# Kernel optimization log

Hardware: AMD Instinct MI355X
Metric: run time of the kernel (lower is better)

The kernel has to match this reference:

```python
import jax, jax.numpy as jnp
import numpy as np

N = 50000      # nodes
E = 800000     # edges
D = 256        # embed_dim
H = 8          # num_heads
HD = D // H    # head_dim = 32
F = 4 * D      # feedforward_dim = 1024
SCALE = D ** -0.5  # note: module scales by embed_dim**-0.5, not head_dim
EPS = 1e-5


def setup_inputs() -> dict:
    key = jax.random.key(0)
    ks = jax.random.split(key, 10)
    x = jax.random.normal(ks[0], (N, D), dtype=jnp.float32)
    edge_indices = jax.random.randint(ks[1], (2, E), 0, N, dtype=jnp.int32)
    s = 0.02
    return {
        "x": x,
        "edge_indices": edge_indices,
        "w_qkv": jax.random.normal(ks[2], (D, 3 * D), dtype=jnp.float32) * s,
        "b_qkv": jnp.zeros((3 * D,), dtype=jnp.float32),
        "ln1_g": jnp.ones((D,), dtype=jnp.float32),
        "ln1_b": jnp.zeros((D,), dtype=jnp.float32),
        "ln2_g": jnp.ones((D,), dtype=jnp.float32),
        "ln2_b": jnp.zeros((D,), dtype=jnp.float32),
        "w1": jax.random.normal(ks[3], (D, F), dtype=jnp.float32) * s,
        "b1": jnp.zeros((F,), dtype=jnp.float32),
        "w2": jax.random.normal(ks[4], (F, D), dtype=jnp.float32) * s,
        "b2": jnp.zeros((D,), dtype=jnp.float32),
    }


def _layer_norm(x, g, b):
    m = jnp.mean(x, axis=-1, keepdims=True)
    v = jnp.mean((x - m) ** 2, axis=-1, keepdims=True)
    return (x - m) * jax.lax.rsqrt(v + EPS) * g + b


def _self_attention(x, edge_indices, w_qkv, b_qkv):
    qkv = (x @ w_qkv + b_qkv).reshape(N, H, 3 * HD)
    q, k, v = qkv[..., :HD], qkv[..., HD:2 * HD], qkv[..., 2 * HD:]
    rows, cols = edge_indices[0], edge_indices[1]
    # per-edge, per-head attention logits: [E, H]
    alpha = jnp.einsum('ehd,ehd->eh', q[rows], k[cols]) * SCALE
    # sparse softmax over each row (destination node) segment
    m = jax.ops.segment_max(alpha, rows, num_segments=N)       # [N, H]
    ea = jnp.exp(alpha - m[rows])                              # [E, H]
    denom = jax.ops.segment_sum(ea, rows, num_segments=N)      # [N, H]
    w = ea / denom[rows]                                       # [E, H]
    # per-head SpMM: out[r] += w_e * v[c]  -> [N, H, HD]
    out = jax.ops.segment_sum(w[:, :, None] * v[cols], rows, num_segments=N)
    return out.reshape(N, D)


def reference(x, edge_indices, w_qkv, b_qkv, ln1_g, ln1_b, ln2_g, ln2_b, w1, b1, w2, b2):
    # post-norm (norm_first=False), dropout=0
    x = _layer_norm(x + _self_attention(x, edge_indices, w_qkv, b_qkv), ln1_g, ln1_b)
    ffn = jax.nn.relu(x @ w1 + b1) @ w2 + b2
    x = _layer_norm(x + ffn, ln2_g, ln2_b)
    return x
```

## Files before the change

kernel.cpp:

```cpp
#include <hip/hip_runtime.h>
#include <hip/hip_bf16.h>

#define N_NODES 50000
#define E_EDGES 800000
#define D_MODEL 256
#define H_HEADS 8
#define HDIM    32
#define F_FFN   1024
#define ATT_SCALE 0.0625f
#define LN_EPS  1e-5f
#define NB_SCAN 196

typedef __attribute__((ext_vector_type(8))) short bf16x8;
typedef __attribute__((ext_vector_type(8))) unsigned short u16x8;
typedef __attribute__((ext_vector_type(4))) float f32x4;

__device__ __forceinline__ float bf2f(__hip_bfloat16 v) { return __bfloat162float(v); }
__device__ __forceinline__ __hip_bfloat16 f2bf(float v) { return __float2bfloat16(v); }
__device__ __forceinline__ unsigned short bfbits(float f) {
    __hip_bfloat16 h = __float2bfloat16(f);
    return *reinterpret_cast<unsigned short*>(&h);
}

__device__ __forceinline__ void unpack_bf8(uint4 u, float* f) {
    f[0] = __uint_as_float(u.x << 16); f[1] = __uint_as_float(u.x & 0xFFFF0000u);
    f[2] = __uint_as_float(u.y << 16); f[3] = __uint_as_float(u.y & 0xFFFF0000u);
    f[4] = __uint_as_float(u.z << 16); f[5] = __uint_as_float(u.z & 0xFFFF0000u);
    f[6] = __uint_as_float(u.w << 16); f[7] = __uint_as_float(u.w & 0xFFFF0000u);
}

template<int CTRL>
__device__ __forceinline__ float dpp_add(float v) {
    int t = __builtin_amdgcn_update_dpp(0, __float_as_int(v), CTRL, 0xF, 0xF, true);
    return v + __int_as_float(t);
}

__device__ __forceinline__ void load_lds16(const void* g, void* l) {
    __builtin_amdgcn_global_load_lds(
        (const __attribute__((address_space(1))) unsigned*)g,
        (__attribute__((address_space(3))) unsigned*)l, 16, 0, 0);
}

#define WAITV(N) asm volatile("s_waitcnt vmcnt(" #N ")" ::: "memory")
#define SBAR()   { __builtin_amdgcn_sched_barrier(0); __builtin_amdgcn_s_barrier(); \
                   __builtin_amdgcn_sched_barrier(0); }


#define PREP_E   E_EDGES
#define PREP_X   3200000
#define PREP_WQ  (768 * 256)
#define PREP_W1  (1024 * 256)
#define PREP_W2  (256 * 1024)
#define PREP_BQ  768
#define PREP_B1  1024
#define PREP_TOT (PREP_E + PREP_X + PREP_WQ + PREP_W1 + PREP_W2 + PREP_BQ + PREP_B1)
__global__ void prep_kernel(const int* __restrict__ rows, unsigned* __restrict__ counts,
                            const float* __restrict__ x, unsigned short* __restrict__ xb,
                            const float* __restrict__ wq, __hip_bfloat16* __restrict__ wtq,
                            const float* __restrict__ w1, __hip_bfloat16* __restrict__ wt1,
                            const float* __restrict__ w2, __hip_bfloat16* __restrict__ wt2,
                            const float* __restrict__ bq, float* __restrict__ bqp,
                            const float* __restrict__ b1, float* __restrict__ b1p) {
    int i = blockIdx.x * blockDim.x + threadIdx.x;
    if (i < PREP_E) {
        atomicAdd(&counts[rows[i]], 1u);
        return;
    }
    i -= PREP_E;
    if (i < PREP_X) {
        float4 v = reinterpret_cast<const float4*>(x)[i];
        ushort4 o;
        o.x = bfbits(v.x); o.y = bfbits(v.y); o.z = bfbits(v.z); o.w = bfbits(v.w);
        reinterpret_cast<ushort4*>(xb)[i] = o;
        return;
    }
    i -= PREP_X;
    if (i < PREP_WQ) {
        int n = i >> 8, k = i & 255;
        int s = n >> 8, prel = n & 255;
        int d = (prel & 192) + ((prel & 15) << 2) + ((prel >> 4) & 3);
        int co = (d >> 5) * 96 + s * 32 + (d & 31);
        wtq[i] = f2bf(wq[(size_t)k * 768 + co]);
        return;
    }
    i -= PREP_WQ;
    if (i < PREP_W1) {
        int n = i >> 8, k = i & 255;
        int f = (n & ~63) + ((n & 15) << 2) + ((n >> 4) & 3);
        wt1[i] = f2bf(w1[(size_t)k * 1024 + f]);
        return;
    }
    i -= PREP_W1;
    if (i < PREP_W2) {
        int n = i >> 10, k = i & 1023;
        wt2[i] = f2bf(w2[(size_t)k * 256 + n]);
        return;
    }
    i -= PREP_W2;
    if (i < PREP_BQ) {
        int s = i >> 8, prel = i & 255;
        int d = (prel & 192) + ((prel & 15) << 2) + ((prel >> 4) & 3);
        bqp[i] = bq[(d >> 5) * 96 + s * 32 + (d & 31)];
        return;
    }
    i -= PREP_BQ;
    if (i < PREP_B1) {
        int f = (i & ~63) + ((i & 15) << 2) + ((i >> 4) & 3);
        b1p[i] = b1[f];
        return;
    }
}

template<bool RELU, int EPI, int KT>
__global__ __launch_bounds__(256)
void mfma_gemm(const __hip_bfloat16* __restrict__ A,
               const __hip_bfloat16* __restrict__ Wt,
               const float* __restrict__ bias,
               __hip_bfloat16* __restrict__ outp,
               __hip_bfloat16* __restrict__ qb,
               unsigned char* __restrict__ kv8,
               int M, int Ncols) {
    __shared__ short Al[3][128 * 32];
    __shared__ short Bl[3][128 * 32];
    const int t = threadIdx.x;
    const int wave = t >> 6, lane = t & 63;

    unsigned flat = blockIdx.y * gridDim.x + blockIdx.x;
    unsigned nwg = gridDim.x * gridDim.y;
    unsigned q8 = nwg >> 3, r8 = nwg & 7;
    unsigned xcd = flat & 7, pos = flat >> 3;
    unsigned wg = (xcd < r8) ? (xcd * (q8 + 1) + pos)
                             : (r8 * (q8 + 1) + (xcd - r8) * q8 + pos);
    const int m0 = (int)(wg / gridDim.x) * 128;
    const int n0 = (int)(wg % gridDim.x) * 128;

    const int wr = wave >> 1, wc = wave & 1;

    const int srow = lane >> 2;
    const int skp  = (lane & 3) ^ ((lane >> 3) & 3);
    const int c0 = wave * 2;
    int ar0 = m0 + c0 * 16 + srow;      if (ar0 >= M) ar0 = M - 1;
    int ar1 = m0 + c0 * 16 + 16 + srow; if (ar1 >= M) ar1 = M - 1;
    const __hip_bfloat16* ga0 = A + (size_t)ar0 * KT + skp * 8;
    const __hip_bfloat16* ga1 = A + (size_t)ar1 * KT + skp * 8;
    const __hip_bfloat16* gb0 = Wt + (size_t)(n0 + c0 * 16 + srow) * KT + skp * 8;
    const __hip_bfloat16* gb1 = Wt + (size_t)(n0 + c0 * 16 + 16 + srow) * KT + skp * 8;

    const int lh = lane & 15, q = lane >> 4;
    const int qs = q ^ ((lane >> 1) & 3);
    const short* faB = &Al[0][(wr * 64 + lh) * 32 + qs * 8];
    const short* fbB = &Bl[0][(wc * 64 + lh) * 32 + qs * 8];

    f32x4 acc[4][4] = {};

#define GSTAGE(B)                                    \
    load_lds16(ga0, &Al[B][c0 * 512]);               \
    load_lds16(ga1, &Al[B][c0 * 512 + 512]);         \
    load_lds16(gb0, &Bl[B][c0 * 512]);               \
    load_lds16(gb1, &Bl[B][c0 * 512 + 512]);         \
    ga0 += 32; ga1 += 32; gb0 += 32; gb1 += 32;

#define GSTEP(FA, FB)                                                       \
    {                                                                       \
        bf16x8 af[4], bfr[4];                                               \
        _Pragma("unroll")                                                   \
        for (int i = 0; i < 4; i++) {                                       \
            af[i]  = *reinterpret_cast<const bf16x8*>((FA) + i * 16 * 32);  \
            bfr[i] = *reinterpret_cast<const bf16x8*>((FB) + i * 16 * 32);  \
        }                                                                   \
        _Pragma("unroll")                                                   \
        for (int mi = 0; mi < 4; mi++)                                      \
            _Pragma("unroll")                                               \
            for (int nj = 0; nj < 4; nj++)                                  \
                acc[mi][nj] = __builtin_amdgcn_mfma_f32_16x16x32_bf16(      \
                    af[mi], bfr[nj], acc[mi][nj], 0, 0, 0);                 \
    }

    constexpr int ns = KT >> 5;
    GSTAGE(0)
    GSTAGE(1)
#pragma unroll
    for (int s = 0; s < ns; ++s) {
        if (s < ns - 1) { WAITV(4); } else { WAITV(0); }
        SBAR();
        if (s + 2 < ns) {
            switch ((s + 2) % 3) {
                case 0: { GSTAGE(0) } break;
                case 1: { GSTAGE(1) } break;
                default: { GSTAGE(2) } break;
            }
        }
        const short* fa = faB + (s % 3) * 4096;
        const short* fb = fbB + (s % 3) * 4096;
        GSTEP(fa, fb)
    }
#undef GSTAGE
#undef GSTEP

    const int B = n0 + wc * 64;
    const int gnbase = B + lh;
    float bv[4];
#pragma unroll
    for (int nj = 0; nj < 4; nj++) bv[nj] = bias[gnbase + nj * 16];

    if (EPI == 0) {
        const int sec = B >> 8;
        const int c = ((B & 255) >> 6) * 16 + lh;
#pragma unroll
        for (int mi = 0; mi < 4; mi++) {
            int gmb = m0 + wr * 64 + mi * 16 + q * 4;
#pragma unroll
            for (int r = 0; r < 4; r++) {
                int gm = gmb + r;
                if (gm >= M) continue;
                float v0 = acc[mi][0][r] + bv[0];
                float v1 = acc[mi][1][r] + bv[1];
                float v2 = acc[mi][2][r] + bv[2];
                float v3 = acc[mi][3][r] + bv[3];
                if (sec == 0) {
                    ushort4 o;
                    o.x = bfbits(v0); o.y = bfbits(v1); o.z = bfbits(v2); o.w = bfbits(v3);
                    *reinterpret_cast<ushort4*>(qb + (size_t)gm * 256 + c * 4) = o;
                } else {
                    unsigned u = (unsigned)__builtin_amdgcn_cvt_pk_fp8_f32(v0, v1, 0, false);
                    u = (unsigned)__builtin_amdgcn_cvt_pk_fp8_f32(v2, v3, (int)u, true);
                    *reinterpret_cast<unsigned*>(
                        kv8 + (size_t)gm * 512 + c * 8 + (sec == 1 ? 0 : 4)) = u;
                }
            }
        }
    } else {
        const int cb = B + lh * 4;
#pragma unroll
        for (int mi = 0; mi < 4; mi++) {
            int gmb = m0 + wr * 64 + mi * 16 + q * 4;
#pragma unroll
            for (int r = 0; r < 4; r++) {
                int gm = gmb + r;
                if (gm >= M) continue;
                float v0 = acc[mi][0][r] + bv[0];
                float v1 = acc[mi][1][r] + bv[1];
                float v2 = acc[mi][2][r] + bv[2];
                float v3 = acc[mi][3][r] + bv[3];
                if (RELU) {
                    v0 = fmaxf(v0, 0.f); v1 = fmaxf(v1, 0.f);
                    v2 = fmaxf(v2, 0.f); v3 = fmaxf(v3, 0.f);
                }
                ushort4 o;
                o.x = bfbits(v0); o.y = bfbits(v1); o.z = bfbits(v2); o.w = bfbits(v3);
                *reinterpret_cast<ushort4*>(outp + (size_t)gm * Ncols + cb) = o;
            }
        }
    }
}

__global__ __launch_bounds__(512)
void ffn2_ln_kernel(const __hip_bfloat16* __restrict__ A,
                    const __hip_bfloat16* __restrict__ Wt,
                    const float* __restrict__ bias,
                    const __hip_bfloat16* __restrict__ resid,
                    const float* __restrict__ g, const float* __restrict__ bb,
                    float* __restrict__ out, int M) {
    __shared__ short LDS[2][(64 + 256) * 32];
    const int t = threadIdx.x;
    const int wave = t >> 6, lane = t & 63;
    const int m0 = blockIdx.x * 64;
    const int wr = wave >> 2, wc = wave & 3;

    const int srow = lane >> 2;
    const int skp  = (lane & 3) ^ ((lane >> 3) & 3);

    const __hip_bfloat16* gsrc0; int loff0;
    const __hip_bfloat16* gsrc1; int loff1;
    const __hip_bfloat16* gsrc2; int loff2;
    {
#define STAGE_INIT(GS, LO, C)                                            \
        if ((C) < 4) {                                                   \
            int r_ = m0 + (C) * 16 + srow; if (r_ >= M) r_ = M - 1;      \
            GS = A + (size_t)r_ * 1024 + skp * 8;                        \
            LO = (C) * 512;                                              \
        } else {                                                         \
            GS = Wt + (size_t)(((C) - 4) * 16 + srow) * 1024 + skp * 8;  \
            LO = 2048 + ((C) - 4) * 512;                                 \
        }
        STAGE_INIT(gsrc0, loff0, wave)
        STAGE_INIT(gsrc1, loff1, wave + 8)
        int c2 = (wave < 4) ? wave + 16 : 16;
        STAGE_INIT(gsrc2, loff2, c2)
#undef STAGE_INIT
    }

    const int lh = lane & 15, q = lane >> 4;
    const int qs = q ^ ((lane >> 1) & 3);
    const short* fa0 = &LDS[0][(wr * 32 + lh) * 32 + qs * 8];
    const short* fb0 = &LDS[0][2048 + (wc * 64 + lh) * 32 + qs * 8];
    const short* fa1 = &LDS[1][(wr * 32 + lh) * 32 + qs * 8];
    const short* fb1 = &LDS[1][2048 + (wc * 64 + lh) * 32 + qs * 8];

    f32x4 acc[2][4] = {};

#define FFN2_STAGE(BUF)                                      \
    load_lds16(gsrc0, &LDS[BUF][loff0]);                     \
    load_lds16(gsrc1, &LDS[BUF][loff1]);                     \
    if (wave < 4) load_lds16(gsrc2, &LDS[BUF][loff2]);       \
    gsrc0 += 32; gsrc1 += 32; gsrc2 += 32;

#define FFN2_STEP(FA, FB)                                                   \
    {                                                                       \
        bf16x8 af[2], bfr[4];                                               \
        _Pragma("unroll")                                                   \
        for (int i = 0; i < 2; i++)                                         \
            af[i] = *reinterpret_cast<const bf16x8*>((FA) + i * 16 * 32);   \
        _Pragma("unroll")                                                   \
        for (int i = 0; i < 4; i++)                                         \
            bfr[i] = *reinterpret_cast<const bf16x8*>((FB) + i * 16 * 32);  \
        _Pragma("unroll")                                                   \
        for (int mi = 0; mi < 2; mi++)                                      \
            _Pragma("unroll")                                               \
            for (int nj = 0; nj < 4; nj++)                                  \
                acc[mi][nj] = __builtin_amdgcn_mfma_f32_16x16x32_bf16(      \
                    af[mi], bfr[nj], acc[mi][nj], 0, 0, 0);                 \
    }

    FFN2_STAGE(0)
    __syncthreads();

    for (int s = 0; s < 32; s += 2) {
        FFN2_STAGE(1)
        FFN2_STEP(fa0, fb0)
        __syncthreads();
        if (s < 30) { FFN2_STAGE(0) }
        FFN2_STEP(fa1, fb1)
        __syncthreads();
    }
#undef FFN2_STAGE
#undef FFN2_STEP

    const int colbase = wc * 64 + lh;
    float bv[4], gv[4], bbv[4];
#pragma unroll
    for (int nj = 0; nj < 4; nj++) {
        bv[nj]  = bias[colbase + nj * 16];
        gv[nj]  = g[colbase + nj * 16];
        bbv[nj] = bb[colbase + nj * 16];
    }

    float ps[2][4], pq[2][4];
#pragma unroll
    for (int mi = 0; mi < 2; mi++) {
#pragma unroll
        for (int r = 0; r < 4; r++) {
            int gm = m0 + wr * 32 + mi * 16 + q * 4 + r;
            int rgm = (gm < M) ? gm : M - 1;
            float s = 0.f, s2 = 0.f;
#pragma unroll
            for (int nj = 0; nj < 4; nj++) {
                float v = acc[mi][nj][r] + bv[nj]
                        + bf2f(resid[(size_t)rgm * 256 + colbase + nj * 16]);
                acc[mi][nj][r] = v;
                s += v; s2 += v * v;
            }
            ps[mi][r] = s; pq[mi][r] = s2;
        }
    }
#pragma unroll
    for (int off = 1; off <= 8; off <<= 1) {
#pragma unroll
        for (int mi = 0; mi < 2; mi++)
#pragma unroll
            for (int r = 0; r < 4; r++) {
                ps[mi][r] += __shfl_xor(ps[mi][r], off);
                pq[mi][r] += __shfl_xor(pq[mi][r], off);
            }
    }
    float* rs = (float*)(&LDS[0][0]);
    float* rq = rs + 256;
    if (lh == 0) {
#pragma unroll
        for (int mi = 0; mi < 2; mi++)
#pragma unroll
            for (int r = 0; r < 4; r++) {
                int m = wr * 32 + mi * 16 + q * 4 + r;
                rs[m * 4 + wc] = ps[mi][r];
                rq[m * 4 + wc] = pq[mi][r];
            }
    }
    __syncthreads();

#pragma unroll
    for (int mi = 0; mi < 2; mi++) {
#pragma unroll
        for (int r = 0; r < 4; r++) {
            int m = wr * 32 + mi * 16 + q * 4 + r;
            int gm = m0 + m;
            if (gm >= M) continue;
            float4 rsv = *reinterpret_cast<const float4*>(&rs[m * 4]);
            float4 rqv = *reinterpret_cast<const float4*>(&rq[m * 4]);
            float S  = (rsv.x + rsv.y) + (rsv.z + rsv.w);
            float S2 = (rqv.x + rqv.y) + (rqv.z + rqv.w);
            float mean = S * (1.f / (float)D_MODEL);
            float var  = S2 * (1.f / (float)D_MODEL) - mean * mean;
            float inv  = rsqrtf(var + LN_EPS);
#pragma unroll
            for (int nj = 0; nj < 4; nj++)
                out[(size_t)gm * 256 + colbase + nj * 16] =
                    (acc[mi][nj][r] - mean) * inv * gv[nj] + bbv[nj];
        }
    }
}

__global__ void scan_blk_kernel(const unsigned* __restrict__ counts,
                                unsigned* __restrict__ offs, unsigned* __restrict__ bsum) {
    __shared__ unsigned sh[256];
    int t = threadIdx.x;
    int i = blockIdx.x * 256 + t;
    unsigned v = (i < N_NODES) ? counts[i] : 0u;
    sh[t] = v;
    __syncthreads();
#pragma unroll
    for (int off = 1; off < 256; off <<= 1) {
        unsigned u = (t >= off) ? sh[t - off] : 0u;
        __syncthreads();
        sh[t] += u;
        __syncthreads();
    }
    if (i < N_NODES) offs[i] = sh[t] - v;
    if (t == 255) bsum[blockIdx.x] = sh[255];
}

__global__ void scan_top_kernel(const unsigned* __restrict__ bsum, unsigned* __restrict__ bpre) {
    __shared__ unsigned sh[256];
    int t = threadIdx.x;
    unsigned v = (t < NB_SCAN) ? bsum[t] : 0u;
    sh[t] = v;
    __syncthreads();
#pragma unroll
    for (int off = 1; off < 256; off <<= 1) {
        unsigned u = (t >= off) ? sh[t - off] : 0u;
        __syncthreads();
        sh[t] += u;
        __syncthreads();
    }
    if (t < NB_SCAN) bpre[t] = sh[t] - v;
    if (t == NB_SCAN - 1) bpre[NB_SCAN] = sh[t];
}

__global__ void scatter_kernel(const int* __restrict__ rows, const int* __restrict__ cols,
                               const unsigned* __restrict__ offsets,
                               const unsigned* __restrict__ bpre,
                               unsigned* __restrict__ cursor,
                               int* __restrict__ scol) {
    int e = blockIdx.x * blockDim.x + threadIdx.x;
    if (e >= E_EDGES) return;
    int r = rows[e];
    unsigned idx = atomicAdd(&cursor[r], 1u);
    scol[offsets[r] + bpre[r >> 8] + idx] = cols[e];
}

__global__ __launch_bounds__(128)
void att_agg_kernel(const __hip_bfloat16* __restrict__ qb,
                    const unsigned char* __restrict__ kv8,
                    const unsigned* __restrict__ offsets,
                    const unsigned* __restrict__ bpre,
                    const int* __restrict__ scol,
                    const __hip_bfloat16* __restrict__ xres,
                    const float* __restrict__ g, const float* __restrict__ bb,
                    __hip_bfloat16* __restrict__ xn) {
    int n = blockIdx.x * 2 + (threadIdx.x >> 6);
    if (n >= N_NODES) return;
    const int lam = threadIdx.x & 63;
    const int hl  = lam & 31;
    const int sel = lam >> 5;
    const unsigned hlb = hl * 16;
    unsigned beg = offsets[n] + bpre[n >> 8];
    unsigned end = (n + 1 == N_NODES) ? bpre[NB_SCAN]
                                      : offsets[n + 1] + bpre[(n + 1) >> 8];

    float qv[8];
    {
        uint4 u = *reinterpret_cast<const uint4*>(qb + (size_t)n * 256 + hl * 8);
        unpack_bf8(u, qv);
#pragma unroll
        for (int i = 0; i < 8; i++) qv[i] *= ATT_SCALE;
    }

    float acc[8] = {};
    float l = 0.f;

#define PAIR_BODY(W, VMUL)                                                      \
    {                                                                           \
        auto k01 = __builtin_amdgcn_cvt_pk_f32_fp8((int)(W).x, false);          \
        auto k23 = __builtin_amdgcn_cvt_pk_f32_fp8((int)(W).x, true);           \
        auto k45 = __builtin_amdgcn_cvt_pk_f32_fp8((int)(W).z, false);          \
        auto k67 = __builtin_amdgcn_cvt_pk_f32_fp8((int)(W).z, true);           \
        float sv = qv[0] * k01[0] + qv[1] * k01[1] + qv[2] * k23[0]             \
                 + qv[3] * k23[1] + qv[4] * k45[0] + qv[5] * k45[1]             \
                 + qv[6] * k67[0] + qv[7] * k67[1];                             \
        sv = dpp_add<0xB1>(sv);                                                 \
        sv = dpp_add<0x4E>(sv);                                                 \
        float pv = __expf(sv) * (VMUL);                                         \
        l += pv;                                                                \
        auto v01 = __builtin_amdgcn_cvt_pk_f32_fp8((int)(W).y, false);          \
        auto v23 = __builtin_amdgcn_cvt_pk_f32_fp8((int)(W).y, true);           \
        auto v45 = __builtin_amdgcn_cvt_pk_f32_fp8((int)(W).w, false);          \
        auto v67 = __builtin_amdgcn_cvt_pk_f32_fp8((int)(W).w, true);           \
        acc[0] += pv * v01[0]; acc[1] += pv * v01[1];                           \
        acc[2] += pv * v23[0]; acc[3] += pv * v23[1];                           \
        acc[4] += pv * v45[0]; acc[5] += pv * v45[1];                           \
        acc[6] += pv * v67[0]; acc[7] += pv * v67[1];                           \
    }

    unsigned e = beg;
    unsigned oA = 0, oB = 0, oC = 0, oD = 0;
    if (e + 8 <= end) {
        oA = ((unsigned)scol[e + sel])     << 9;
        oB = ((unsigned)scol[e + 2 + sel]) << 9;
        oC = ((unsigned)scol[e + 4 + sel]) << 9;
        oD = ((unsigned)scol[e + 6 + sel]) << 9;
    }
    while (e + 8 <= end) {
        uint4 wa = *reinterpret_cast<const uint4*>(kv8 + (oA + hlb));
        uint4 wb = *reinterpret_cast<const uint4*>(kv8 + (oB + hlb));
        uint4 wc = *reinterpret_cast<const uint4*>(kv8 + (oC + hlb));
        uint4 wd = *reinterpret_cast<const uint4*>(kv8 + (oD + hlb));
        e += 8;
        if (e + 8 <= end) {
            oA = ((unsigned)scol[e + sel])     << 9;
            oB = ((unsigned)scol[e + 2 + sel]) << 9;
            oC = ((unsigned)scol[e + 4 + sel]) << 9;
            oD = ((unsigned)scol[e + 6 + sel]) << 9;
        }
        PAIR_BODY(wa, 1.0f)
        PAIR_BODY(wb, 1.0f)
        PAIR_BODY(wc, 1.0f)
        PAIR_BODY(wd, 1.0f)
    }
    for (; e + 2 <= end; e += 2) {
        unsigned o0 = ((unsigned)scol[e + sel]) << 9;
        uint4 wa = *reinterpret_cast<const uint4*>(kv8 + (o0 + hlb));
        PAIR_BODY(wa, 1.0f)
    }
    if (e < end) {
        unsigned o0 = ((unsigned)scol[e]) << 9;
        uint4 wa = *reinterpret_cast<const uint4*>(kv8 + (o0 + hlb));
        PAIR_BODY(wa, sel ? 0.0f : 1.0f)
    }
#undef PAIR_BODY

    l += __shfl_xor(l, 32);
#pragma unroll
    for (int i = 0; i < 8; i++) acc[i] += __shfl_xor(acc[i], 32);

    float inv_l = (l > 0.f) ? 1.f / l : 0.f;

    float tv[8];
    {
        float xv[8];
        uint4 u = *reinterpret_cast<const uint4*>(xres + (size_t)n * D_MODEL + hl * 8);
        unpack_bf8(u, xv);
#pragma unroll
        for (int i = 0; i < 8; i++) tv[i] = acc[i] * inv_l + xv[i];
    }

    float s = 0.f, s2 = 0.f;
#pragma unroll
    for (int i = 0; i < 8; i++) { s += tv[i]; s2 += tv[i] * tv[i]; }
#pragma unroll
    for (int off = 1; off <= 16; off <<= 1) {
        s  += __shfl_xor(s, off);
        s2 += __shfl_xor(s2, off);
    }
    float mean = s * (1.f / (float)D_MODEL);
    float var  = s2 * (1.f / (float)D_MODEL) - mean * mean;
    float inv  = rsqrtf(var + LN_EPS);

    if (sel == 0) {
        const float4* gp = reinterpret_cast<const float4*>(g);
        const float4* bp = reinterpret_cast<const float4*>(bb);
        float4 g0 = gp[hl * 2], g1 = gp[hl * 2 + 1];
        float4 b0 = bp[hl * 2], b1 = bp[hl * 2 + 1];
        float gv[8] = {g0.x, g0.y, g0.z, g0.w, g1.x, g1.y, g1.z, g1.w};
        float bv[8] = {b0.x, b0.y, b0.z, b0.w, b1.x, b1.y, b1.z, b1.w};
        u16x8 o;
#pragma unroll
        for (int i = 0; i < 8; i++)
            o[i] = bfbits((tv[i] - mean) * inv * gv[i] + bv[i]);
        *reinterpret_cast<u16x8*>(xn + (size_t)n * D_MODEL + hl * 8) = o;
    }
}

extern "C" void kernel_launch(void* const* d_in, const int* in_sizes, int n_in,
                              void* d_out, int out_size, void* d_ws, size_t ws_size,
                              hipStream_t stream) {
    const float* x     = (const float*)d_in[0];
    const int*   ei    = (const int*)d_in[1];
    const float* w_qkv = (const float*)d_in[2];
    const float* b_qkv = (const float*)d_in[3];
    const float* ln1_g = (const float*)d_in[4];
    const float* ln1_b = (const float*)d_in[5];
    const float* ln2_g = (const float*)d_in[6];
    const float* ln2_b = (const float*)d_in[7];
    const float* w1    = (const float*)d_in[8];
    const float* b1    = (const float*)d_in[9];
    const float* w2    = (const float*)d_in[10];
    const float* b2    = (const float*)d_in[11];
    const int* rows = ei;
    const int* cols = ei + E_EDGES;

    char* ws = (char*)d_ws;
    __hip_bfloat16* qb      = (__hip_bfloat16*)(ws + 0);
    unsigned char*  kv8     = (unsigned char*)(ws + 25600000);
    __hip_bfloat16* hbuf    = (__hip_bfloat16*)(ws + 0);
    __hip_bfloat16* xb      = (__hip_bfloat16*)(ws + 102400000);
    __hip_bfloat16* wtq     = (__hip_bfloat16*)(ws + 128000000);
    __hip_bfloat16* wt1     = (__hip_bfloat16*)(ws + 128400000);
    __hip_bfloat16* wt2     = (__hip_bfloat16*)(ws + 129000000);
    unsigned*       counts  = (unsigned*)(ws + 129600000);
    unsigned*       offsets = (unsigned*)(ws + 129800000);
    unsigned*       cursor  = (unsigned*)(ws + 130000008);
    int*            scol    = (int*)(ws + 130200008);
    unsigned*       bsum    = (unsigned*)(ws + 133400008);
    unsigned*       bpre    = (unsigned*)(ws + 133401032);
    float*          bqp     = (float*)(ws + 133500000);
    float*          b1p     = (float*)(ws + 133510000);
    __hip_bfloat16* xn      = (__hip_bfloat16*)(ws + 153600000);

    const int nbM = (N_NODES + 127) / 128;

    hipMemsetAsync(counts, 0, N_NODES * sizeof(unsigned), stream);
    hipMemsetAsync(cursor, 0, N_NODES * sizeof(unsigned), stream);

    prep_kernel<<<(PREP_TOT + 255) / 256, 256, 0, stream>>>(
        rows, counts, x, (unsigned short*)xb, w_qkv, wtq, w1, wt1, w2, wt2,
        b_qkv, bqp, b1, b1p);

    mfma_gemm<false, 0, 256><<<dim3(768 / 128, nbM), 256, 0, stream>>>(
        xb, wtq, bqp, nullptr, qb, kv8, N_NODES, 768);

    scan_blk_kernel<<<NB_SCAN, 256, 0, stream>>>(counts, offsets, bsum);
    scan_top_kernel<<<1, 256, 0, stream>>>(bsum, bpre);
    scatter_kernel<<<(E_EDGES + 255) / 256, 256, 0, stream>>>(rows, cols, offsets, bpre,
                                                              cursor, scol);

    att_agg_kernel<<<(N_NODES + 1) / 2, 128, 0, stream>>>(qb, kv8, offsets, bpre, scol,
                                                          xb, ln1_g, ln1_b, xn);

    mfma_gemm<true, 1, 256><<<dim3(F_FFN / 128, nbM), 256, 0, stream>>>(
        xn, wt1, b1p, hbuf, nullptr, nullptr, N_NODES, F_FFN);

    ffn2_ln_kernel<<<(N_NODES + 63) / 64, 512, 0, stream>>>(hbuf, wt2, b2, xn, ln2_g, ln2_b,
                                                            (float*)d_out, N_NODES);
}
```

Before: 414.9 us.

## Merge QKV GEMM, edge scatter and FFN weight transposes into one launch

Folds the two-level scan into a single kernel: the last block to finish, picked by an atomic ticket, computes the block prefixes. A heterogeneous mega-kernel then runs the QKV GEMM tiles, the CSR edge scatter and LDS-tiled transposes of the FFN weights as different block ranges of one grid. W1/W2 conversion moves out of the scalar prep kernel into coalesced tiled transposes. This removes several launches and lets independent work overlap, at the cost of scatter blocks needing the full 48KB LDS allocation and a more complex kernel.

```diff
diff --git a/kernel.cpp b/kernel.cpp
--- a/kernel.cpp
+++ b/kernel.cpp
@@ -49,18 +49,13 @@
 #define PREP_E   E_EDGES
 #define PREP_X   3200000
 #define PREP_WQ  (768 * 256)
-#define PREP_W1  (1024 * 256)
-#define PREP_W2  (256 * 1024)
 #define PREP_BQ  768
-#define PREP_B1  1024
-#define PREP_TOT (PREP_E + PREP_X + PREP_WQ + PREP_W1 + PREP_W2 + PREP_BQ + PREP_B1)
+#define PREP_TOT (PREP_E + PREP_X + PREP_WQ + PREP_BQ + 1)
 __global__ void prep_kernel(const int* __restrict__ rows, unsigned* __restrict__ counts,
                             const float* __restrict__ x, unsigned short* __restrict__ xb,
                             const float* __restrict__ wq, __hip_bfloat16* __restrict__ wtq,
-                            const float* __restrict__ w1, __hip_bfloat16* __restrict__ wt1,
-                            const float* __restrict__ w2, __hip_bfloat16* __restrict__ wt2,
                             const float* __restrict__ bq, float* __restrict__ bqp,
-                            const float* __restrict__ b1, float* __restrict__ b1p) {
+                            unsigned* __restrict__ scnt) {
     int i = blockIdx.x * blockDim.x + threadIdx.x;
     if (i < PREP_E) {
         atomicAdd(&counts[rows[i]], 1u);
@@ -84,19 +79,6 @@
         return;
     }
     i -= PREP_WQ;
-    if (i < PREP_W1) {
-        int n = i >> 8, k = i & 255;
-        int f = (n & ~63) + ((n & 15) << 2) + ((n >> 4) & 3);
-        wt1[i] = f2bf(w1[(size_t)k * 1024 + f]);
-        return;
-    }
-    i -= PREP_W1;
-    if (i < PREP_W2) {
-        int n = i >> 10, k = i & 1023;
-        wt2[i] = f2bf(w2[(size_t)k * 256 + n]);
-        return;
-    }
-    i -= PREP_W2;
     if (i < PREP_BQ) {
         int s = i >> 8, prel = i & 255;
         int d = (prel & 192) + ((prel & 15) << 2) + ((prel >> 4) & 3);
@@ -104,47 +86,145 @@
         return;
     }
     i -= PREP_BQ;
-    if (i < PREP_B1) {
-        int f = (i & ~63) + ((i & 15) << 2) + ((i >> 4) & 3);
-        b1p[i] = b1[f];
-        return;
-    }
-}
-
-template<bool RELU, int EPI, int KT>
+    if (i == 0) *scnt = 0u;
+}
+
+__global__ void scan_blk_kernel(const unsigned* __restrict__ counts,
+                                unsigned* __restrict__ offs, unsigned* __restrict__ bsum,
+                                unsigned* __restrict__ bpre, unsigned* __restrict__ scnt) {
+    __shared__ unsigned sh[256];
+    __shared__ unsigned lastflag;
+    int t = threadIdx.x;
+    int i = blockIdx.x * 256 + t;
+    unsigned v = (i < N_NODES) ? counts[i] : 0u;
+    sh[t] = v;
+    __syncthreads();
+#pragma unroll
+    for (int off = 1; off < 256; off <<= 1) {
+        unsigned u = (t >= off) ? sh[t - off] : 0u;
+        __syncthreads();
+        sh[t] += u;
+        __syncthreads();
+    }
+    if (i < N_NODES) offs[i] = sh[t] - v;
+    if (t == 255) {
+        bsum[blockIdx.x] = sh[255];
+        __threadfence();
+        unsigned ticket = atomicAdd(scnt, 1u);
+        lastflag = (ticket == NB_SCAN - 1) ? 1u : 0u;
+    }
+    __syncthreads();
+    if (lastflag) {
+        __threadfence();
+        unsigned v2 = (t < NB_SCAN) ? atomicAdd(&bsum[t], 0u) : 0u;
+        __syncthreads();
+        sh[t] = v2;
+        __syncthreads();
+#pragma unroll
+        for (int off = 1; off < 256; off <<= 1) {
+            unsigned u = (t >= off) ? sh[t - off] : 0u;
+            __syncthreads();
+            sh[t] += u;
+            __syncthreads();
+        }
+        if (t < NB_SCAN) bpre[t] = sh[t] - v2;
+        if (t == NB_SCAN - 1) bpre[NB_SCAN] = sh[t];
+    }
+}
+
+#define NB_QKV_X 6
+#define NB_QKV_Y ((N_NODES + 127) / 128)
+#define NB_QKV   (NB_QKV_X * NB_QKV_Y)
+#define NB_SCAT  ((E_EDGES + 255) / 256)
+#define NB_TRANS 128
+#define NB_MEGA  (NB_QKV + NB_SCAT + NB_TRANS + 1)
 __global__ __launch_bounds__(256)
-void mfma_gemm(const __hip_bfloat16* __restrict__ A,
-               const __hip_bfloat16* __restrict__ Wt,
-               const float* __restrict__ bias,
-               __hip_bfloat16* __restrict__ outp,
-               __hip_bfloat16* __restrict__ qb,
-               unsigned char* __restrict__ kv8,
-               int M, int Ncols) {
+void mega_kernel(const __hip_bfloat16* __restrict__ A,
+                 const __hip_bfloat16* __restrict__ Wt,
+                 const float* __restrict__ bias,
+                 __hip_bfloat16* __restrict__ qb,
+                 unsigned char* __restrict__ kv8,
+                 const int* __restrict__ rows, const int* __restrict__ cols,
+                 const unsigned* __restrict__ offsets, const unsigned* __restrict__ bpre,
+                 unsigned* __restrict__ cursor, int* __restrict__ scol,
+                 const float* __restrict__ w1, __hip_bfloat16* __restrict__ wt1,
+                 const float* __restrict__ w2, __hip_bfloat16* __restrict__ wt2,
+                 const float* __restrict__ b1, float* __restrict__ b1p,
+                 int M) {
     __shared__ short Al[3][128 * 32];
     __shared__ short Bl[3][128 * 32];
+    const int bid = blockIdx.x;
     const int t = threadIdx.x;
+
+    if (bid >= NB_QKV) {
+        int rb = bid - NB_QKV;
+        if (rb < NB_SCAT) {
+            int e = rb * 256 + t;
+            if (e < E_EDGES) {
+                int r = rows[e];
+                unsigned idx = atomicAdd(&cursor[r], 1u);
+                scol[offsets[r] + bpre[r >> 8] + idx] = cols[e];
+            }
+            return;
+        }
+        rb -= NB_SCAT;
+        if (rb < NB_TRANS) {
+            float* tl = reinterpret_cast<float*>(&Al[0][0]);
+            const float* src; __hip_bfloat16* dst;
+            int k0, c0, W, KD; bool perm;
+            if (rb < 64) {
+                int kt = rb >> 4, ct = rb & 15;
+                k0 = kt * 64; c0 = ct * 64; W = 1024; KD = 256;
+                src = w1; dst = wt1; perm = true;
+            } else {
+                int rb2 = rb - 64;
+                int kt = rb2 >> 2, ct = rb2 & 3;
+                k0 = kt * 64; c0 = ct * 64; W = 256; KD = 1024;
+                src = w2; dst = wt2; perm = false;
+            }
+#pragma unroll
+            for (int r = 0; r < 16; ++r) {
+                int idx = r * 256 + t;
+                int kk = idx >> 6, cc = idx & 63;
+                tl[kk * 65 + cc] = src[(size_t)(k0 + kk) * W + c0 + cc];
+            }
+            __syncthreads();
+#pragma unroll
+            for (int r = 0; r < 16; ++r) {
+                int idx = r * 256 + t;
+                int nl = idx >> 6, kk = idx & 63;
+                int cl = perm ? (((nl & 15) << 2) + ((nl >> 4) & 3)) : nl;
+                dst[(size_t)(c0 + nl) * KD + k0 + kk] = f2bf(tl[kk * 65 + cl]);
+            }
+            return;
+        }
+        for (int j = t; j < 1024; j += 256) {
+            int f = (j & ~63) + ((j & 15) << 2) + ((j >> 4) & 3);
+            b1p[j] = b1[f];
+        }
+        return;
+    }
+
     const int wave = t >> 6, lane = t & 63;
-
-    unsigned flat = blockIdx.y * gridDim.x + blockIdx.x;
-    unsigned nwg = gridDim.x * gridDim.y;
+    unsigned flat = (unsigned)bid;
+    unsigned nwg = NB_QKV;
     unsigned q8 = nwg >> 3, r8 = nwg & 7;
     unsigned xcd = flat & 7, pos = flat >> 3;
     unsigned wg = (xcd < r8) ? (xcd * (q8 + 1) + pos)
                              : (r8 * (q8 + 1) + (xcd - r8) * q8 + pos);
-    const int m0 = (int)(wg / gridDim.x) * 128;
-    const int n0 = (int)(wg % gridDim.x) * 128;
+    const int m0 = (int)(wg / NB_QKV_X) * 128;
+    const int n0 = (int)(wg % NB_QKV_X) * 128;
 
     const int wr = wave >> 1, wc = wave & 1;
-
     const int srow = lane >> 2;
     const int skp  = (lane & 3) ^ ((lane >> 3) & 3);
     const int c0 = wave * 2;
     int ar0 = m0 + c0 * 16 + srow;      if (ar0 >= M) ar0 = M - 1;
     int ar1 = m0 + c0 * 16 + 16 + srow; if (ar1 >= M) ar1 = M - 1;
-    const __hip_bfloat16* ga0 = A + (size_t)ar0 * KT + skp * 8;
-    const __hip_bfloat16* ga1 = A + (size_t)ar1 * KT + skp * 8;
-    const __hip_bfloat16* gb0 = Wt + (size_t)(n0 + c0 * 16 + srow) * KT + skp * 8;
-    const __hip_bfloat16* gb1 = Wt + (size_t)(n0 + c0 * 16 + 16 + srow) * KT + skp * 8;
+    const __hip_bfloat16* ga0 = A + (size_t)ar0 * 256 + skp * 8;
+    const __hip_bfloat16* ga1 = A + (size_t)ar1 * 256 + skp * 8;
+    const __hip_bfloat16* gb0 = Wt + (size_t)(n0 + c0 * 16 + srow) * 256 + skp * 8;
+    const __hip_bfloat16* gb1 = Wt + (size_t)(n0 + c0 * 16 + 16 + srow) * 256 + skp * 8;
 
     const int lh = lane & 15, q = lane >> 4;
     const int qs = q ^ ((lane >> 1) & 3);
@@ -176,6 +256,121 @@
                     af[mi], bfr[nj], acc[mi][nj], 0, 0, 0);                 \
     }
 
+    GSTAGE(0)
+    GSTAGE(1)
+#pragma unroll
+    for (int s = 0; s < 8; ++s) {
+        if (s < 7) { WAITV(4); } else { WAITV(0); }
+        SBAR();
+        if (s + 2 < 8) {
+            switch ((s + 2) % 3) {
+                case 0: { GSTAGE(0) } break;
+                case 1: { GSTAGE(1) } break;
+                default: { GSTAGE(2) } break;
+            }
+        }
+        const short* fa = faB + (s % 3) * 4096;
+        const short* fb = fbB + (s % 3) * 4096;
+        GSTEP(fa, fb)
+    }
+#undef GSTAGE
+#undef GSTEP
+
+    const int B = n0 + wc * 64;
+    const int gnbase = B + lh;
+    float bv[4];
+#pragma unroll
+    for (int nj = 0; nj < 4; nj++) bv[nj] = bias[gnbase + nj * 16];
+
+    const int sec = B >> 8;
+    const int c = ((B & 255) >> 6) * 16 + lh;
+#pragma unroll
+    for (int mi = 0; mi < 4; mi++) {
+        int gmb = m0 + wr * 64 + mi * 16 + q * 4;
+#pragma unroll
+        for (int r = 0; r < 4; r++) {
+            int gm = gmb + r;
+            if (gm >= M) continue;
+            float v0 = acc[mi][0][r] + bv[0];
+            float v1 = acc[mi][1][r] + bv[1];
+            float v2 = acc[mi][2][r] + bv[2];
+            float v3 = acc[mi][3][r] + bv[3];
+            if (sec == 0) {
+                ushort4 o;
+                o.x = bfbits(v0); o.y = bfbits(v1); o.z = bfbits(v2); o.w = bfbits(v3);
+                *reinterpret_cast<ushort4*>(qb + (size_t)gm * 256 + c * 4) = o;
+            } else {
+                unsigned u = (unsigned)__builtin_amdgcn_cvt_pk_fp8_f32(v0, v1, 0, false);
+                u = (unsigned)__builtin_amdgcn_cvt_pk_fp8_f32(v2, v3, (int)u, true);
+                *reinterpret_cast<unsigned*>(
+                    kv8 + (size_t)gm * 512 + c * 8 + (sec == 1 ? 0 : 4)) = u;
+            }
+        }
+    }
+}
+
+template<bool RELU, int EPI, int KT>
+__global__ __launch_bounds__(256)
+void mfma_gemm(const __hip_bfloat16* __restrict__ A,
+               const __hip_bfloat16* __restrict__ Wt,
+               const float* __restrict__ bias,
+               __hip_bfloat16* __restrict__ outp,
+               int M, int Ncols) {
+    __shared__ short Al[3][128 * 32];
+    __shared__ short Bl[3][128 * 32];
+    const int t = threadIdx.x;
+    const int wave = t >> 6, lane = t & 63;
+
+    unsigned flat = blockIdx.y * gridDim.x + blockIdx.x;
+    unsigned nwg = gridDim.x * gridDim.y;
+    unsigned q8 = nwg >> 3, r8 = nwg & 7;
+    unsigned xcd = flat & 7, pos = flat >> 3;
+    unsigned wg = (xcd < r8) ? (xcd * (q8 + 1) + pos)
+                             : (r8 * (q8 + 1) + (xcd - r8) * q8 + pos);
+    const int m0 = (int)(wg / gridDim.x) * 128;
+    const int n0 = (int)(wg % gridDim.x) * 128;
+
+    const int wr = wave >> 1, wc = wave & 1;
+    const int srow = lane >> 2;
+    const int skp  = (lane & 3) ^ ((lane >> 3) & 3);
+    const int c0 = wave * 2;
+    int ar0 = m0 + c0 * 16 + srow;      if (ar0 >= M) ar0 = M - 1;
+    int ar1 = m0 + c0 * 16 + 16 + srow; if (ar1 >= M) ar1 = M - 1;
+    const __hip_bfloat16* ga0 = A + (size_t)ar0 * KT + skp * 8;
+    const __hip_bfloat16* ga1 = A + (size_t)ar1 * KT + skp * 8;
+    const __hip_bfloat16* gb0 = Wt + (size_t)(n0 + c0 * 16 + srow) * KT + skp * 8;
+    const __hip_bfloat16* gb1 = Wt + (size_t)(n0 + c0 * 16 + 16 + srow) * KT + skp * 8;
+
+    const int lh = lane & 15, q = lane >> 4;
+    const int qs = q ^ ((lane >> 1) & 3);
+    const short* faB = &Al[0][(wr * 64 + lh) * 32 + qs * 8];
+    const short* fbB = &Bl[0][(wc * 64 + lh) * 32 + qs * 8];
+
+    f32x4 acc[4][4] = {};
+
+#define GSTAGE(B)                                    \
+    load_lds16(ga0, &Al[B][c0 * 512]);               \
+    load_lds16(ga1, &Al[B][c0 * 512 + 512]);         \
+    load_lds16(gb0, &Bl[B][c0 * 512]);               \
+    load_lds16(gb1, &Bl[B][c0 * 512 + 512]);         \
+    ga0 += 32; ga1 += 32; gb0 += 32; gb1 += 32;
+
+#define GSTEP(FA, FB)                                                       \
+    {                                                                       \
+        bf16x8 af[4], bfr[4];                                               \
+        _Pragma("unroll")                                                   \
+        for (int i = 0; i < 4; i++) {                                       \
+            af[i]  = *reinterpret_cast<const bf16x8*>((FA) + i * 16 * 32);  \
+            bfr[i] = *reinterpret_cast<const bf16x8*>((FB) + i * 16 * 32);  \
+        }                                                                   \
+        _Pragma("unroll")                                                   \
+        for (int mi = 0; mi < 4; mi++)                                      \
+            _Pragma("unroll")                                               \
+            for (int nj = 0; nj < 4; nj++)                                  \
+                acc[mi][nj] = __builtin_amdgcn_mfma_f32_16x16x32_bf16(      \
+                    af[mi], bfr[nj], acc[mi][nj], 0, 0, 0);                 \
+    }
+
     constexpr int ns = KT >> 5;
     GSTAGE(0)
     GSTAGE(1)
@@ -203,53 +398,25 @@
 #pragma unroll
     for (int nj = 0; nj < 4; nj++) bv[nj] = bias[gnbase + nj * 16];
 
-    if (EPI == 0) {
-        const int sec = B >> 8;
-        const int c = ((B & 255) >> 6) * 16 + lh;
-#pragma unroll
-        for (int mi = 0; mi < 4; mi++) {
-            int gmb = m0 + wr * 64 + mi * 16 + q * 4;
-#pragma unroll
-            for (int r = 0; r < 4; r++) {
-                int gm = gmb + r;
-                if (gm >= M) continue;
-                float v0 = acc[mi][0][r] + bv[0];
-                float v1 = acc[mi][1][r] + bv[1];
-                float v2 = acc[mi][2][r] + bv[2];
-                float v3 = acc[mi][3][r] + bv[3];
-                if (sec == 0) {
-                    ushort4 o;
-                    o.x = bfbits(v0); o.y = bfbits(v1); o.z = bfbits(v2); o.w = bfbits(v3);
-                    *reinterpret_cast<ushort4*>(qb + (size_t)gm * 256 + c * 4) = o;
-                } else {
-                    unsigned u = (unsigned)__builtin_amdgcn_cvt_pk_fp8_f32(v0, v1, 0, false);
-                    u = (unsigned)__builtin_amdgcn_cvt_pk_fp8_f32(v2, v3, (int)u, true);
-                    *reinterpret_cast<unsigned*>(
-                        kv8 + (size_t)gm * 512 + c * 8 + (sec == 1 ? 0 : 4)) = u;
-                }
-            }
-        }
-    } else {
-        const int cb = B + lh * 4;
-#pragma unroll
-        for (int mi = 0; mi < 4; mi++) {
-            int gmb = m0 + wr * 64 + mi * 16 + q * 4;
-#pragma unroll
-            for (int r = 0; r < 4; r++) {
-                int gm = gmb + r;
-                if (gm >= M) continue;
-                float v0 = acc[mi][0][r] + bv[0];
-                float v1 = acc[mi][1][r] + bv[1];
-                float v2 = acc[mi][2][r] + bv[2];
-                float v3 = acc[mi][3][r] + bv[3];
-                if (RELU) {
-                    v0 = fmaxf(v0, 0.f); v1 = fmaxf(v1, 0.f);
-                    v2 = fmaxf(v2, 0.f); v3 = fmaxf(v3, 0.f);
-                }
-                ushort4 o;
-                o.x = bfbits(v0); o.y = bfbits(v1); o.z = bfbits(v2); o.w = bfbits(v3);
-                *reinterpret_cast<ushort4*>(outp + (size_t)gm * Ncols + cb) = o;
-            }
+    const int cb = B + lh * 4;
+#pragma unroll
+    for (int mi = 0; mi < 4; mi++) {
+        int gmb = m0 + wr * 64 + mi * 16 + q * 4;
+#pragma unroll
+        for (int r = 0; r < 4; r++) {
+            int gm = gmb + r;
+            if (gm >= M) continue;
+            float v0 = acc[mi][0][r] + bv[0];
+            float v1 = acc[mi][1][r] + bv[1];
+            float v2 = acc[mi][2][r] + bv[2];
+            float v3 = acc[mi][3][r] + bv[3];
+            if (RELU) {
+                v0 = fmaxf(v0, 0.f); v1 = fmaxf(v1, 0.f);
+                v2 = fmaxf(v2, 0.f); v3 = fmaxf(v3, 0.f);
+            }
+            ushort4 o;
+            o.x = bfbits(v0); o.y = bfbits(v1); o.z = bfbits(v2); o.w = bfbits(v3);
+            *reinterpret_cast<ushort4*>(outp + (size_t)gm * Ncols + cb) = o;
         }
     }
 }
@@ -407,54 +574,6 @@
                     (acc[mi][nj][r] - mean) * inv * gv[nj] + bbv[nj];
         }
     }
-}
-
-__global__ void scan_blk_kernel(const unsigned* __restrict__ counts,
-                                unsigned* __restrict__ offs, unsigned* __restrict__ bsum) {
-    __shared__ unsigned sh[256];
-    int t = threadIdx.x;
-    int i = blockIdx.x * 256 + t;
-    unsigned v = (i < N_NODES) ? counts[i] : 0u;
-    sh[t] = v;
-    __syncthreads();
-#pragma unroll
-    for (int off = 1; off < 256; off <<= 1) {
-        unsigned u = (t >= off) ? sh[t - off] : 0u;
-        __syncthreads();
-        sh[t] += u;
-        __syncthreads();
-    }
-    if (i < N_NODES) offs[i] = sh[t] - v;
-    if (t == 255) bsum[blockIdx.x] = sh[255];
-}
-
-__global__ void scan_top_kernel(const unsigned* __restrict__ bsum, unsigned* __restrict__ bpre) {
-    __shared__ unsigned sh[256];
-    int t = threadIdx.x;
-    unsigned v = (t < NB_SCAN) ? bsum[t] : 0u;
-    sh[t] = v;
-    __syncthreads();
-#pragma unroll
-    for (int off = 1; off < 256; off <<= 1) {
-        unsigned u = (t >= off) ? sh[t - off] : 0u;
-        __syncthreads();
-        sh[t] += u;
-        __syncthreads();
-    }
-    if (t < NB_SCAN) bpre[t] = sh[t] - v;
-    if (t == NB_SCAN - 1) bpre[NB_SCAN] = sh[t];
-}
-
-__global__ void scatter_kernel(const int* __restrict__ rows, const int* __restrict__ cols,
-                               const unsigned* __restrict__ offsets,
-                               const unsigned* __restrict__ bpre,
-                               unsigned* __restrict__ cursor,
-                               int* __restrict__ scol) {
-    int e = blockIdx.x * blockDim.x + threadIdx.x;
-    if (e >= E_EDGES) return;
-    int r = rows[e];
-    unsigned idx = atomicAdd(&cursor[r], 1u);
-    scol[offsets[r] + bpre[r >> 8] + idx] = cols[e];
 }
 
 __global__ __launch_bounds__(128)
@@ -624,6 +743,7 @@
     float*          bqp     = (float*)(ws + 133500000);
     float*          b1p     = (float*)(ws + 133510000);
     __hip_bfloat16* xn      = (__hip_bfloat16*)(ws + 153600000);
+    unsigned*       scnt    = bsum + 200;
 
     const int nbM = (N_NODES + 127) / 128;
 
@@ -631,22 +751,20 @@
     hipMemsetAsync(cursor, 0, N_NODES * sizeof(unsigned), stream);
 
     prep_kernel<<<(PREP_TOT + 255) / 256, 256, 0, stream>>>(
-        rows, counts, x, (unsigned short*)xb, w_qkv, wtq, w1, wt1, w2, wt2,
-        b_qkv, bqp, b1, b1p);
-
-    mfma_gemm<false, 0, 256><<<dim3(768 / 128, nbM), 256, 0, stream>>>(
-        xb, wtq, bqp, nullptr, qb, kv8, N_NODES, 768);
-
-    scan_blk_kernel<<<NB_SCAN, 256, 0, stream>>>(counts, offsets, bsum);
-    scan_top_kernel<<<1, 256, 0, stream>>>(bsum, bpre);
-    scatter_kernel<<<(E_EDGES + 255) / 256, 256, 0, stream>>>(rows, cols, offsets, bpre,
-                                                              cursor, scol);
+        rows, counts, x, (unsigned short*)xb, w_qkv, wtq, b_qkv, bqp, scnt);
+
+    scan_blk_kernel<<<NB_SCAN, 256, 0, stream>>>(counts, offsets, bsum, bpre, scnt);
+
+    mega_kernel<<<NB_MEGA, 256, 0, stream>>>(
+        xb, wtq, bqp, qb, kv8,
+        rows, cols, offsets, bpre, cursor, scol,
+        w1, wt1, w2, wt2, b1, b1p, N_NODES);
 
     att_agg_kernel<<<(N_NODES + 1) / 2, 128, 0, stream>>>(qb, kv8, offsets, bpre, scol,
                                                           xb, ln1_g, ln1_b, xn);
 
     mfma_gemm<true, 1, 256><<<dim3(F_FFN / 128, nbM), 256, 0, stream>>>(
-        xn, wt1, b1p, hbuf, nullptr, nullptr, N_NODES, F_FFN);
+        xn, wt1, b1p, hbuf, N_NODES, F_FFN);
 
     ffn2_ln_kernel<<<(N_NODES + 63) / 64, 512, 0, stream>>>(hbuf, wt2, b2, xn, ln2_g, ln2_b,
                                                             (float*)d_out, N_NODES);
```

After: 411.2 us. No clear change (-0.9%).
